# Optimization experiments

Measured on AMD Instinct MI355X. Metric: run time of the kernel, lower is better.

Reference implementation:

```python
import jax, jax.numpy as jnp
import numpy as np

T_ITERS = 48  # number of unrolled PDHG iterations (init kwarg T)


def _grad3(u):
    """Forward-difference gradient with circular BC.
    u: (P, 1, X, Y, T) -> (P, 3, X, Y, T).
    conv with kernel (0,-1,1) + circular pad == roll(v,-1,axis) - v."""
    v = u[:, 0]
    return jnp.stack([jnp.roll(v, -1, axis=a) - v for a in (1, 2, 3)], axis=1)


def _grad3_adj(q):
    """Adjoint (negative divergence) with circular BC.
    q: (P, 3, X, Y, T) -> (P, 1, X, Y, T)."""
    out = sum(jnp.roll(q[:, d], 1, axis=d + 1) - q[:, d] for d in range(3))
    return out[:, None]


def setup_inputs() -> dict:
    key = jax.random.key(0)
    k1, k2 = jax.random.split(key)
    x = jax.random.normal(k1, (2, 1, 160, 160, 16), dtype=jnp.float32)
    # positive per-voxel regularization map, one per gradient direction
    lambda_map = jax.random.uniform(k2, (2, 3, 160, 160, 16), dtype=jnp.float32)
    return {"x": x, "lambda_map": lambda_map}


def reference(x, lambda_map):
    # op_norm_AHA = 1, op_norm_GHG = sqrt(12) -> L = sqrt(1 + 12)
    L = jnp.sqrt(jnp.asarray(13.0, x.dtype))
    s10 = jax.nn.sigmoid(jnp.asarray(10.0, x.dtype))  # sigmoid of init value 10.0
    sigma = s10 / L
    tau = s10 / L
    theta = s10

    xnoisy = x
    p = x
    q = jnp.zeros((x.shape[0], 3) + x.shape[2:], dtype=x.dtype)
    x0 = x
    xbar = x

    def step(carry, _):
        p, q, x0, xbar = carry
        p = (p + sigma * (xbar - xnoisy)) / (1.0 + sigma)
        q = jnp.clip(q + sigma * _grad3(xbar), -lambda_map, lambda_map)
        x1 = x0 - tau * p - tau * _grad3_adj(q)
        xbar = x1 + theta * (x1 - x0)
        return (p, q, x1, xbar), None

    (p, q, x1, xbar), _ = jax.lax.scan(step, (p, q, x0, xbar), None, length=T_ITERS)
    return x1
```

## Files before the change

kernel.cpp:

```cpp
#include <hip/hip_runtime.h>
#include <math.h>

#define XDIM 160
#define YDIM 160
#define TDIM 16
#define NB 2
#define T_ITERS 48
#define TILE 10
#define R1S 16
#define R0S 18
#define TPT (XDIM / TILE)
#define NTHR 512
#define NTHRP 1024
#define NGRP (T_ITERS / 4)
#define FLAG_STRIDE 16

constexpr int VOL  = XDIM * YDIM * TDIM;
constexpr int NX   = NB * VOL;
constexpr int NBLK = NB * TPT * TPT;

constexpr int Q0B = R0S * R0S * TDIM;
constexpr int Q1B = Q0B + 17 * 16 * TDIM;
constexpr int SLDS = Q1B + 16 * 17 * TDIM;

typedef _Float16 hreal;
typedef _Float16 half4 __attribute__((ext_vector_type(4)));

__device__ __forceinline__ float clampl(float v, float l) {
    return fminf(fmaxf(v, -l), l);
}
__device__ __forceinline__ int wrap(int v) {
    return v < 0 ? v + XDIM : (v >= XDIM ? v - XDIM : v);
}
__device__ __forceinline__ int wrapT(int v) {
    return v < 0 ? v + TPT : (v >= TPT ? v - TPT : v);
}
__device__ __forceinline__ void ld4(const float* p, float* d) {
    float4 v = *(const float4*)p;
    d[0] = v.x; d[1] = v.y; d[2] = v.z; d[3] = v.w;
}
__device__ __forceinline__ void st4(float* p, const float* s) {
    *(float4*)p = make_float4(s[0], s[1], s[2], s[3]);
}
__device__ __forceinline__ void h2f4(const hreal* p, float* d) {
    half4 v = *(const half4*)p;
    d[0] = (float)v.x; d[1] = (float)v.y; d[2] = (float)v.z; d[3] = (float)v.w;
}
__device__ __forceinline__ float qrot_up(float x) {
    return __int_as_float(__builtin_amdgcn_update_dpp(
        0, __float_as_int(x), 0x39, 0xF, 0xF, true));
}
__device__ __forceinline__ float qrot_dn(float x) {
    return __int_as_float(__builtin_amdgcn_update_dpp(
        0, __float_as_int(x), 0x93, 0xF, 0xF, true));
}

__global__ __launch_bounds__(256) void init_kernel(
    const float* __restrict__ x, const float* __restrict__ lam,
    float* __restrict__ pA, float* __restrict__ xA,
    hreal* __restrict__ famA,
    hreal* __restrict__ lamh, hreal* __restrict__ xnh,
    unsigned* __restrict__ flags)
{
    int i = blockIdx.x * blockDim.x + threadIdx.x;
    if (i < NX) {
        float v = x[i];
        pA[i] = v; xA[i] = v;
        famA[i] = (hreal)v;
        xnh[i]  = (hreal)v;
    }
    if (i < 3 * NX) {
        famA[NX + i] = (hreal)0.f;
        lamh[i] = (hreal)lam[i];
    }
    if (flags && i < NBLK * FLAG_STRIDE) flags[i] = 0u;
}

__global__ __launch_bounds__(NTHRP, 8) void pd_persist(
    const hreal* __restrict__ xnh, const hreal* __restrict__ lamh,
    float* __restrict__ pA, float* __restrict__ pB,
    float* __restrict__ xA, float* __restrict__ xB,
    hreal* __restrict__ famA, hreal* __restrict__ famB,
    unsigned* __restrict__ flags,
    float sigma, float inv1ps, float tau, float theta)
{
    __shared__ float S[SLDS];

    const int tid = threadIdx.x;
    const int region = blockIdx.x & 7;
    const int local  = blockIdx.x >> 3;
    const int b  = region >> 2;
    const int tx = ((region >> 1) & 1) * 8 + (local >> 3);
    const int ty = (region & 1) * 8 + (local & 7);
    const int X0 = tx * TILE, Y0 = ty * TILE;
    const int t0 = (tid & 3) * 4;
    const int QD = NX + 2 * b * VOL;

    const int myFlag = (b * TPT * TPT + tx * TPT + ty) * FLAG_STRIDE;
    const unsigned* nbFlag = nullptr;
    if (tid < 8) {
        const int dxs[8] = {-1,-1,-1, 0, 0, 1, 1, 1};
        const int dys[8] = {-1, 0, 1,-1, 1,-1, 0, 1};
        int nx = wrapT(tx + dxs[tid]);
        int ny = wrapT(ty + dys[tid]);
        nbFlag = flags + (b * TPT * TPT + nx * TPT + ny) * FLAG_STRIDE;
    }

    const int line = tid >> 2;
    const int lx = line >> 4, ly = line & 15;

    float p[4], xv[4], q2[4];
    float xb[4], q0[4], q1[4];
    half4 XNr, L0r, L1r, L2r;

    const int gx0 = wrap(X0 - 3 + lx), gy0 = wrap(Y0 - 3 + ly);
    const int ro = b * VOL + (gx0 * YDIM + gy0) * TDIM + t0;
    const int so = b * VOL + ((X0 + lx - 3) * YDIM + (Y0 + ly - 3)) * TDIM + t0;
    const int a_xb  = ((lx + 1) * R0S + (ly + 1)) * TDIM + t0;
    const int a_q0w = Q0B + ((lx + 1) * 16 + ly) * TDIM + t0;
    const int a_q1w = Q1B + (lx * 17 + (ly + 1)) * TDIM + t0;
    const bool c_   = lx >= 3 && lx < 13 && ly >= 3 && ly < 13;
    const int ox = lx - 3, oy = ly - 3;
    const bool pxs_ = (ox >= 3 && ox < 7 && oy >= 3 && oy < 7);
    const bool qs_  = (ox >= 4 && ox < 6 && oy >= 4 && oy < 6);
    {
        int qoff = ro + 2 * b * VOL;
        XNr = *(const half4*)(xnh + ro);
        L0r = *(const half4*)(lamh + qoff);
        L1r = *(const half4*)(lamh + qoff + VOL);
        L2r = *(const half4*)(lamh + qoff + 2 * VOL);
    }
    half4 LRr;
    int rQ = 0, rXBC = 0;
    if (tid < 64) {
        int rly = tid >> 2;
        LRr = *(const half4*)(lamh + b * 3 * VOL +
              (wrap(X0 - 4) * YDIM + wrap(Y0 - 3 + rly)) * TDIM + t0);
        rQ   = Q0B + rly * TDIM + t0;
        rXBC = (rly + 1) * TDIM + t0;
    } else if (tid < 128) {
        int rlx = (tid - 64) >> 2;
        LRr = *(const half4*)(lamh + b * 3 * VOL + VOL +
              (wrap(X0 - 3 + rlx) * YDIM + wrap(Y0 - 4)) * TDIM + t0);
        rQ   = Q1B + (rlx * 17) * TDIM + t0;
        rXBC = ((rlx + 1) * R0S) * TDIM + t0;
    }

    #pragma unroll 1
    for (int g = 0; g < NGRP; ++g) {
        const bool e = (g & 1) == 0;
        const bool first = (g == 0);
        const bool fin   = (g == NGRP - 1);
        const float* __restrict__ pIn  = e ? pA : pB;
        float* __restrict__ pOut       = e ? pB : pA;
        const float* __restrict__ xIn  = e ? xA : xB;
        float* __restrict__ xOut       = e ? xB : xA;
        const hreal* __restrict__ famIn = e ? famA : famB;
        hreal* __restrict__ famOut      = e ? famB : famA;

        if (!first) {
            if (tid < 8) {
                const unsigned tgt = (unsigned)g;
                for (unsigned it = 0; it < (1u << 22); ++it) {
                    if (__hip_atomic_load(nbFlag, __ATOMIC_ACQUIRE,
                                          __HIP_MEMORY_SCOPE_AGENT) >= tgt)
                        break;
                    __builtin_amdgcn_s_sleep(1);
                }
            }
            __syncthreads();
            __threadfence();
        }

        for (int s = tid; s < R0S * R0S * 4; s += NTHRP) {
            int sq = s & 3, ln = s >> 2;
            int rx = ln / R0S, ry = ln % R0S;
            if (!first && rx >= 4 && rx < 14 && ry >= 4 && ry < 14) continue;
            int gx = wrap(X0 - 4 + rx), gy = wrap(Y0 - 4 + ry);
            float v[4];
            h2f4(famIn + b * VOL + (gx * YDIM + gy) * TDIM + sq * 4, v);
            st4(S + ln * TDIM + sq * 4, v);
        }
        for (int s = tid; s < 17 * 16 * 4; s += NTHRP) {
            int sq = s & 3, ln = s >> 2;
            int sx = ln / 16, sy = ln % 16;
            if (!first && sx >= 3 && sx < 14 && sy >= 3 && sy < 13) continue;
            int gx = wrap(X0 - 4 + sx), gy = wrap(Y0 - 3 + sy);
            float v[4];
            h2f4(famIn + NX + b * 3 * VOL + (gx * YDIM + gy) * TDIM + sq * 4, v);
            st4(S + Q0B + ln * TDIM + sq * 4, v);
        }
        for (int s = tid; s < 16 * 17 * 4; s += NTHRP) {
            int sq = s & 3, ln = s >> 2;
            int sx = ln / 17, sy = ln % 17;
            if (!first && sx >= 3 && sx < 13 && sy >= 3 && sy < 14) continue;
            int gx = wrap(X0 - 3 + sx), gy = wrap(Y0 - 4 + sy);
            float v[4];
            h2f4(famIn + NX + b * 3 * VOL + VOL + (gx * YDIM + gy) * TDIM + sq * 4, v);
            st4(S + Q1B + ln * TDIM + sq * 4, v);
        }

        if (first || !c_) {
            ld4(pIn + ro, p);
            ld4(xIn + ro, xv);
            h2f4(famIn + ro + QD + 2 * VOL, q2);
        }
        __syncthreads();

        ld4(S + a_xb, xb);

        #pragma unroll
        for (int k = 1; k <= 4; ++k) {
            const int lo = k - 1, hi = 17 - k;

            if (k == 1) {
                if (tid < 64) {
                    float qr[4], xbc[4], xpr[4];
                    ld4(S + rQ, qr);
                    ld4(S + rXBC, xbc);
                    ld4(S + rXBC + R0S * TDIM, xpr);
                    #pragma unroll
                    for (int j = 0; j < 4; ++j)
                        qr[j] = clampl(qr[j] + sigma * (xpr[j] - xbc[j]), (float)LRr[j]);
                    st4(S + rQ, qr);
                } else if (tid < 128) {
                    float qr[4], xbc[4], xpr[4];
                    ld4(S + rQ, qr);
                    ld4(S + rXBC, xbc);
                    ld4(S + rXBC + TDIM, xpr);
                    #pragma unroll
                    for (int j = 0; j < 4; ++j)
                        qr[j] = clampl(qr[j] + sigma * (xpr[j] - xbc[j]), (float)LRr[j]);
                    st4(S + rQ, qr);
                }
            }

            float xpx[4], xpy[4];
            if (k == 1) {
                ld4(S + a_q0w, q0);
                ld4(S + a_q1w, q1);
            }
            ld4(S + a_xb + R0S * TDIM, xpx);
            ld4(S + a_xb + TDIM,       xpy);
            {
                bool inX = (lx >= lo && lx < hi), inY = (ly >= lo && ly < hi);
                bool aq0 = inY && (lx >= lo - 1) && (lx < hi);
                bool aq1 = inX && (ly >= lo - 1) && (ly < hi);
                if (aq0) {
                    #pragma unroll
                    for (int j = 0; j < 4; ++j)
                        q0[j] = clampl(q0[j] + sigma * (xpx[j] - xb[j]),
                                       (float)L0r[j]);
                    st4(S + a_q0w, q0);
                }
                if (aq1) {
                    #pragma unroll
                    for (int j = 0; j < 4; ++j)
                        q1[j] = clampl(q1[j] + sigma * (xpy[j] - xb[j]),
                                       (float)L1r[j]);
                    st4(S + a_q1w, q1);
                }
            }
            __syncthreads();

            float q0b[4], q1b[4];
            ld4(S + a_q0w - 16 * TDIM, q0b);
            ld4(S + a_q1w - TDIM,      q1b);
            {
                bool ax = (lx >= lo && lx < hi && ly >= lo && ly < hi);
                if (ax) {
                    float xb_tp = qrot_up(xb[0]);
                    #pragma unroll
                    for (int j = 0; j < 4; ++j) {
                        float gt = ((j < 3) ? xb[j + 1] : xb_tp) - xb[j];
                        q2[j] = clampl(q2[j] + sigma * gt, (float)L2r[j]);
                        p[j]  = (p[j] + sigma * (xb[j] - (float)XNr[j]))
                                * inv1ps;
                    }

                    float q2tm = qrot_dn(q2[3]);
                    #pragma unroll
                    for (int j = 0; j < 4; ++j) {
                        float q2p = (j == 0) ? q2tm : q2[j - 1];
                        float div = (q0b[j] - q0[j]) + (q1b[j] - q1[j])
                                  + (q2p - q2[j]);
                        float xnew = xv[j] - tau * (p[j] + div);
                        xb[j] = xnew + theta * (xnew - xv[j]);
                        xv[j] = xnew;
                    }
                    st4(S + a_xb, xb);
                }
            }
            if (k < 4) __syncthreads();
        }

        if (c_) {
            if (fin) {
                st4(xOut + so, xv);
            } else {
                if (!pxs_) {
                    st4(pOut + so, p);
                    st4(xOut + so, xv);
                }
                if (!qs_) {
                    half4 h;
                    h.x = (hreal)xb[0]; h.y = (hreal)xb[1];
                    h.z = (hreal)xb[2]; h.w = (hreal)xb[3];
                    *(half4*)(famOut + so) = h;
                    h.x = (hreal)q0[0]; h.y = (hreal)q0[1];
                    h.z = (hreal)q0[2]; h.w = (hreal)q0[3];
                    *(half4*)(famOut + so + QD) = h;
                    h.x = (hreal)q1[0]; h.y = (hreal)q1[1];
                    h.z = (hreal)q1[2]; h.w = (hreal)q1[3];
                    *(half4*)(famOut + so + QD + VOL) = h;
                    h.x = (hreal)q2[0]; h.y = (hreal)q2[1];
                    h.z = (hreal)q2[2]; h.w = (hreal)q2[3];
                    *(half4*)(famOut + so + QD + 2 * VOL) = h;
                }
            }
        }

        if (!fin) {
            __threadfence();
            __syncthreads();
            if (tid == 0)
                __hip_atomic_store(flags + myFlag, (unsigned)(g + 1),
                                   __ATOMIC_RELEASE, __HIP_MEMORY_SCOPE_AGENT);
        }
    }
}

__global__ __launch_bounds__(NTHR, 4) void pd_step4(
    const hreal* __restrict__ xnh, const hreal* __restrict__ lamh,
    const float* __restrict__ pIn, float* __restrict__ pOut,
    const float* __restrict__ xIn, float* __restrict__ xOut,
    const hreal* __restrict__ xbIn, hreal* __restrict__ xbOut,
    const hreal* __restrict__ qIn, hreal* __restrict__ qOut,
    float sigma, float inv1ps, float tau, float theta)
{
    __shared__ float xbS[R0S * R0S * TDIM];
    __shared__ float q0S[17 * 16 * TDIM];
    __shared__ float q1S[16 * 17 * TDIM];

    const int tid = threadIdx.x;
    const int b   = blockIdx.x / (TPT * TPT);
    const int rem = blockIdx.x % (TPT * TPT);
    const int X0  = (rem / TPT) * TILE;
    const int Y0  = (rem % TPT) * TILE;
    const int xbase = b * VOL, qbase = b * 3 * VOL;

    const int qd = tid & 3, t0 = qd * 4;
    const int lane  = tid & 63;
    const int upSrc = (lane & 60) | ((lane + 1) & 3);
    const int dnSrc = (lane & 60) | ((lane + 3) & 3);

    for (int s = tid; s < R0S * R0S * 4; s += NTHR) {
        int sq = s & 3, ln = s >> 2;
        int rx = ln / R0S, ry = ln % R0S;
        int gx = wrap(X0 - 4 + rx), gy = wrap(Y0 - 4 + ry);
        float v[4];
        h2f4(xbIn + xbase + (gx * YDIM + gy) * TDIM + sq * 4, v);
        st4(xbS + ln * TDIM + sq * 4, v);
    }
    for (int s = tid; s < 17 * 16 * 4; s += NTHR) {
        int sq = s & 3, ln = s >> 2;
        int sx = ln / 16, sy = ln % 16;
        int gx = wrap(X0 - 4 + sx), gy = wrap(Y0 - 3 + sy);
        float v[4];
        h2f4(qIn + qbase + (gx * YDIM + gy) * TDIM + sq * 4, v);
        st4(q0S + ln * TDIM + sq * 4, v);
    }
    for (int s = tid; s < 16 * 17 * 4; s += NTHR) {
        int sq = s & 3, ln = s >> 2;
        int sx = ln / 17, sy = ln % 17;
        int gx = wrap(X0 - 3 + sx), gy = wrap(Y0 - 4 + sy);
        float v[4];
        h2f4(qIn + qbase + VOL + (gx * YDIM + gy) * TDIM + sq * 4, v);
        st4(q1S + ln * TDIM + sq * 4, v);
    }

    float p[2][4], xv[2][4], xb[2][4], q0[2][4], q1[2][4], q2[2][4];
    half4 XNr[2], L0r[2], L1r[2], L2r[2];
    #pragma unroll
    for (int m = 0; m < 2; ++m) {
        int line = 128 * m + (tid >> 2);
        int lx = line >> 4, ly = line & 15;
        int gx = wrap(X0 - 3 + lx), gy = wrap(Y0 - 3 + ly);
        int off  = xbase + (gx * YDIM + gy) * TDIM + t0;
        int qoff = qbase + (gx * YDIM + gy) * TDIM + t0;
        ld4(pIn + off, p[m]);
        ld4(xIn + off, xv[m]);
        h2f4(qIn + qoff + 2 * VOL, q2[m]);
        XNr[m] = *(const half4*)(xnh + off);
        L0r[m] = *(const half4*)(lamh + qoff);
        L1r[m] = *(const half4*)(lamh + qoff + VOL);
        L2r[m] = *(const half4*)(lamh + qoff + 2 * VOL);
    }

    half4 LRr;
    if (tid < 64) {
        int rly = tid >> 2;
        LRr = *(const half4*)(lamh + qbase +
              (wrap(X0 - 4) * YDIM + wrap(Y0 - 3 + rly)) * TDIM + t0);
    } else if (tid < 128) {
        int rlx = (tid - 64) >> 2;
        LRr = *(const half4*)(lamh + qbase + VOL +
              (wrap(X0 - 3 + rlx) * YDIM + wrap(Y0 - 4)) * TDIM + t0);
    }

    __syncthreads();

    #pragma unroll
    for (int m = 0; m < 2; ++m) {
        int line = 128 * m + (tid >> 2);
        int lx = line >> 4, ly = line & 15;
        ld4(xbS + ((lx + 1) * R0S + (ly + 1)) * TDIM + t0, xb[m]);
    }

    #pragma unroll
    for (int k = 1; k <= 4; ++k) {
        const int lo = k - 1, hi = 17 - k;

        if (k == 1) {
            if (tid < 64) {
                int rly = tid >> 2;
                float qr[4], xbc[4], xpx[4];
                ld4(q0S + rly * TDIM + t0, qr);
                ld4(xbS + (rly + 1) * TDIM + t0, xbc);
                ld4(xbS + (R0S + rly + 1) * TDIM + t0, xpx);
                #pragma unroll
                for (int j = 0; j < 4; ++j)
                    qr[j] = clampl(qr[j] + sigma * (xpx[j] - xbc[j]), (float)LRr[j]);
                st4(q0S + rly * TDIM + t0, qr);
            } else if (tid < 128) {
                int rlx = (tid - 64) >> 2;
                float qr[4], xbc[4], xpy[4];
                ld4(q1S + (rlx * 17) * TDIM + t0, qr);
                ld4(xbS + ((rlx + 1) * R0S) * TDIM + t0, xbc);
                ld4(xbS + ((rlx + 1) * R0S + 1) * TDIM + t0, xpy);
                #pragma unroll
                for (int j = 0; j < 4; ++j)
                    qr[j] = clampl(qr[j] + sigma * (xpy[j] - xbc[j]), (float)LRr[j]);
                st4(q1S + (rlx * 17) * TDIM + t0, qr);
            }
        }

        #pragma unroll
        for (int m = 0; m < 2; ++m) {
            int line = 128 * m + (tid >> 2);
            int lx = line >> 4, ly = line & 15;
            bool inX = (lx >= lo && lx < hi), inY = (ly >= lo && ly < hi);
            bool aq0 = inY && (lx >= lo - 1) && (lx < hi);
            bool aq1 = inX && (ly >= lo - 1) && (ly < hi);
            bool ax  = inX && inY;

            if (k == 1) {
                ld4(q0S + ((lx + 1) * 16 + ly) * TDIM + t0, q0[m]);
                ld4(q1S + (lx * 17 + (ly + 1)) * TDIM + t0, q1[m]);
            }
            if (aq0) {
                float xpx[4];
                ld4(xbS + ((lx + 2) * R0S + (ly + 1)) * TDIM + t0, xpx);
                #pragma unroll
                for (int j = 0; j < 4; ++j)
                    q0[m][j] = clampl(q0[m][j] + sigma * (xpx[j] - xb[m][j]),
                                      (float)L0r[m][j]);
                st4(q0S + ((lx + 1) * 16 + ly) * TDIM + t0, q0[m]);
            }
            if (aq1) {
                float xpy[4];
                ld4(xbS + ((lx + 1) * R0S + (ly + 2)) * TDIM + t0, xpy);
                #pragma unroll
                for (int j = 0; j < 4; ++j)
                    q1[m][j] = clampl(q1[m][j] + sigma * (xpy[j] - xb[m][j]),
                                      (float)L1r[m][j]);
                st4(q1S + (lx * 17 + (ly + 1)) * TDIM + t0, q1[m]);
            }
            if (ax) {
                float xb_tp = __shfl(xb[m][0], upSrc, 64);
                #pragma unroll
                for (int j = 0; j < 4; ++j) {
                    float gt = ((j < 3) ? xb[m][j + 1] : xb_tp) - xb[m][j];
                    q2[m][j] = clampl(q2[m][j] + sigma * gt, (float)L2r[m][j]);
                    p[m][j]  = (p[m][j] + sigma * (xb[m][j] - (float)XNr[m][j]))
                               * inv1ps;
                }
            }
        }
        __syncthreads();

        #pragma unroll
        for (int m = 0; m < 2; ++m) {
            int line = 128 * m + (tid >> 2);
            int lx = line >> 4, ly = line & 15;
            bool ax = (lx >= lo && lx < hi && ly >= lo && ly < hi);
            if (ax) {
                float q0b[4], q1b[4];
                ld4(q0S + (lx * 16 + ly) * TDIM + t0, q0b);
                ld4(q1S + (lx * 17 + ly) * TDIM + t0, q1b);
                float q2tm = __shfl(q2[m][3], dnSrc, 64);
                #pragma unroll
                for (int j = 0; j < 4; ++j) {
                    float q2p = (j == 0) ? q2tm : q2[m][j - 1];
                    float div = (q0b[j] - q0[m][j]) + (q1b[j] - q1[m][j])
                              + (q2p - q2[m][j]);
                    float xnew = xv[m][j] - tau * (p[m][j] + div);
                    xb[m][j] = xnew + theta * (xnew - xv[m][j]);
                    xv[m][j] = xnew;
                }
                if (k < 4)
                    st4(xbS + ((lx + 1) * R0S + (ly + 1)) * TDIM + t0, xb[m]);
            }
        }
        if (k < 4) __syncthreads();
    }

    #pragma unroll
    for (int m = 0; m < 2; ++m) {
        int line = 128 * m + (tid >> 2);
        int lx = line >> 4, ly = line & 15;
        if (lx >= 3 && lx < 13 && ly >= 3 && ly < 13) {
            int gx = X0 + lx - 3, gy = Y0 + ly - 3;
            int off  = xbase + (gx * YDIM + gy) * TDIM + t0;
            int qoff = qbase + (gx * YDIM + gy) * TDIM + t0;
            st4(pOut + off, p[m]);
            st4(xOut + off, xv[m]);
            half4 h;
            h.x = (hreal)xb[m][0]; h.y = (hreal)xb[m][1];
            h.z = (hreal)xb[m][2]; h.w = (hreal)xb[m][3];
            *(half4*)(xbOut + off) = h;
            h.x = (hreal)q0[m][0]; h.y = (hreal)q0[m][1];
            h.z = (hreal)q0[m][2]; h.w = (hreal)q0[m][3];
            *(half4*)(qOut + qoff) = h;
            h.x = (hreal)q1[m][0]; h.y = (hreal)q1[m][1];
            h.z = (hreal)q1[m][2]; h.w = (hreal)q1[m][3];
            *(half4*)(qOut + qoff + VOL) = h;
            h.x = (hreal)q2[m][0]; h.y = (hreal)q2[m][1];
            h.z = (hreal)q2[m][2]; h.w = (hreal)q2[m][3];
            *(half4*)(qOut + qoff + 2 * VOL) = h;
        }
    }
}

extern "C" void kernel_launch(void* const* d_in, const int* in_sizes, int n_in,
                              void* d_out, int out_size, void* d_ws, size_t ws_size,
                              hipStream_t stream) {
    const float* x   = (const float*)d_in[0];
    const float* lam = (const float*)d_in[1];
    float* out = (float*)d_out;
    float* ws  = (float*)d_ws;

    float* pA  = ws;
    float* pB  = ws + (size_t)NX;
    float* xBb = ws + (size_t)2 * NX;
    float* xAb = out;
    hreal* hb  = (hreal*)(ws + (size_t)3 * NX);
    hreal* famA = hb;
    hreal* famB = hb + (size_t)4 * NX;
    hreal* lamh = hb + (size_t)8 * NX;
    hreal* xnh  = hb + (size_t)11 * NX;
    unsigned* flags = (unsigned*)(ws + (size_t)9 * NX);

    const size_t ws_need = (size_t)9 * NX * sizeof(float)
                         + (size_t)NBLK * FLAG_STRIDE * sizeof(unsigned);

    const double s10 = 1.0 / (1.0 + exp(-10.0));
    const double L   = sqrt(13.0);
    float sigma  = (float)(s10 / L);
    float tau    = sigma;
    float theta  = (float)s10;
    float inv1ps = (float)(1.0 / (1.0 + s10 / L));

    static int persist_ok = -1;
    if (persist_ok < 0) {
        int nb = 0;
        hipError_t oe = hipOccupancyMaxActiveBlocksPerMultiprocessor(
            &nb, pd_persist, NTHRP, 0);
        persist_ok = (oe == hipSuccess && nb >= 2) ? 1 : 0;
        (void)hipGetLastError();
    }
    const bool use_persist = persist_ok == 1 && ws_size >= ws_need;

    init_kernel<<<(3 * NX + 255) / 256, 256, 0, stream>>>(
        x, lam, pA, xAb, famA, lamh, xnh, use_persist ? flags : nullptr);

    if (use_persist) {
        pd_persist<<<NBLK, NTHRP, 0, stream>>>(
            xnh, lamh, pA, pB, xAb, xBb, famA, famB, flags,
            sigma, inv1ps, tau, theta);
    } else {
        for (int j = 0; j < NGRP; ++j) {
            const bool e = (j & 1) == 0;
            pd_step4<<<NBLK, NTHR, 0, stream>>>(
                xnh, lamh,
                e ? pA : pB,   e ? pB : pA,
                e ? xAb : xBb, e ? xBb : xAb,
                e ? famA : famB, e ? famB : famA,
                e ? famA + NX : famB + NX, e ? famB + NX : famA + NX,
                sigma, inv1ps, tau, theta);
        }
    }
}
```

Measured before the change: 253.3 us.

## Recompute backward q neighbours in registers and double-buffer xbar to halve barriers

```diff
diff --git a/kernel.cpp b/kernel.cpp
--- a/kernel.cpp
+++ b/kernel.cpp
@@ -19,9 +19,8 @@
 constexpr int NX   = NB * VOL;
 constexpr int NBLK = NB * TPT * TPT;
 
-constexpr int Q0B = R0S * R0S * TDIM;
-constexpr int Q1B = Q0B + 17 * 16 * TDIM;
-constexpr int SLDS = Q1B + 16 * 17 * TDIM;
+constexpr int XBN  = R0S * R0S * TDIM;
+constexpr int SLDS = 2 * XBN;
 
 typedef _Float16 hreal;
 typedef _Float16 half4 __attribute__((ext_vector_type(4)));
@@ -85,6 +84,8 @@
     float sigma, float inv1ps, float tau, float theta)
 {
     __shared__ float S[SLDS];
+    float* const Sb0 = S;
+    float* const Sb1 = S + XBN;
 
     const int tid = threadIdx.x;
     const int region = blockIdx.x & 7;
@@ -109,17 +110,19 @@
     const int line = tid >> 2;
     const int lx = line >> 4, ly = line & 15;
 
-    float p[4], xv[4], q2[4];
-    float xb[4], q0[4], q1[4];
-    half4 XNr, L0r, L1r, L2r;
+    float p[4], xv[4], q2[4], xb[4], q0[4], q1[4], q0b[4], q1b[4];
+    half4 XNr, L0r, L1r, L2r, L0b, L1b;
 
     const int gx0 = wrap(X0 - 3 + lx), gy0 = wrap(Y0 - 3 + ly);
-    const int ro = b * VOL + (gx0 * YDIM + gy0) * TDIM + t0;
-    const int so = b * VOL + ((X0 + lx - 3) * YDIM + (Y0 + ly - 3)) * TDIM + t0;
-    const int a_xb  = ((lx + 1) * R0S + (ly + 1)) * TDIM + t0;
-    const int a_q0w = Q0B + ((lx + 1) * 16 + ly) * TDIM + t0;
-    const int a_q1w = Q1B + (lx * 17 + (ly + 1)) * TDIM + t0;
+    const int gxm = wrap(X0 - 4 + lx), gym = wrap(Y0 - 4 + ly);
+    const int ro   = b * VOL + (gx0 * YDIM + gy0) * TDIM + t0;
+    const int rob0 = b * VOL + (gxm * YDIM + gy0) * TDIM + t0;
+    const int rob1 = b * VOL + (gx0 * YDIM + gym) * TDIM + t0;
+    const int so   = b * VOL + ((X0 + lx - 3) * YDIM + (Y0 + ly - 3)) * TDIM + t0;
+    const int a_xb = ((lx + 1) * R0S + (ly + 1)) * TDIM + t0;
     const bool c_   = lx >= 3 && lx < 13 && ly >= 3 && ly < 13;
+    const bool cb0_ = lx >= 4 && lx < 14 && ly >= 3 && ly < 13;
+    const bool cb1_ = lx >= 3 && lx < 13 && ly >= 4 && ly < 14;
     const int ox = lx - 3, oy = ly - 3;
     const bool pxs_ = (ox >= 3 && ox < 7 && oy >= 3 && oy < 7);
     const bool qs_  = (ox >= 4 && ox < 6 && oy >= 4 && oy < 6);
@@ -129,21 +132,8 @@
         L0r = *(const half4*)(lamh + qoff);
         L1r = *(const half4*)(lamh + qoff + VOL);
         L2r = *(const half4*)(lamh + qoff + 2 * VOL);
-    }
-    half4 LRr;
-    int rQ = 0, rXBC = 0;
-    if (tid < 64) {
-        int rly = tid >> 2;
-        LRr = *(const half4*)(lamh + b * 3 * VOL +
-              (wrap(X0 - 4) * YDIM + wrap(Y0 - 3 + rly)) * TDIM + t0);
-        rQ   = Q0B + rly * TDIM + t0;
-        rXBC = (rly + 1) * TDIM + t0;
-    } else if (tid < 128) {
-        int rlx = (tid - 64) >> 2;
-        LRr = *(const half4*)(lamh + b * 3 * VOL + VOL +
-              (wrap(X0 - 3 + rlx) * YDIM + wrap(Y0 - 4)) * TDIM + t0);
-        rQ   = Q1B + (rlx * 17) * TDIM + t0;
-        rXBC = ((rlx + 1) * R0S) * TDIM + t0;
+        L0b = *(const half4*)(lamh + rob0 + 2 * b * VOL);
+        L1b = *(const half4*)(lamh + rob1 + 2 * b * VOL + VOL);
     }
 
     #pragma unroll 1
@@ -179,119 +169,82 @@
             int gx = wrap(X0 - 4 + rx), gy = wrap(Y0 - 4 + ry);
             float v[4];
             h2f4(famIn + b * VOL + (gx * YDIM + gy) * TDIM + sq * 4, v);
-            st4(S + ln * TDIM + sq * 4, v);
-        }
-        for (int s = tid; s < 17 * 16 * 4; s += NTHRP) {
-            int sq = s & 3, ln = s >> 2;
-            int sx = ln / 16, sy = ln % 16;
-            if (!first && sx >= 3 && sx < 14 && sy >= 3 && sy < 13) continue;
-            int gx = wrap(X0 - 4 + sx), gy = wrap(Y0 - 3 + sy);
-            float v[4];
-            h2f4(famIn + NX + b * 3 * VOL + (gx * YDIM + gy) * TDIM + sq * 4, v);
-            st4(S + Q0B + ln * TDIM + sq * 4, v);
-        }
-        for (int s = tid; s < 16 * 17 * 4; s += NTHRP) {
-            int sq = s & 3, ln = s >> 2;
-            int sx = ln / 17, sy = ln % 17;
-            if (!first && sx >= 3 && sx < 13 && sy >= 3 && sy < 14) continue;
-            int gx = wrap(X0 - 3 + sx), gy = wrap(Y0 - 4 + sy);
-            float v[4];
-            h2f4(famIn + NX + b * 3 * VOL + VOL + (gx * YDIM + gy) * TDIM + sq * 4, v);
-            st4(S + Q1B + ln * TDIM + sq * 4, v);
+            st4(Sb0 + ln * TDIM + sq * 4, v);
         }
 
         if (first || !c_) {
             ld4(pIn + ro, p);
             ld4(xIn + ro, xv);
             h2f4(famIn + ro + QD + 2 * VOL, q2);
-        }
+            h2f4(famIn + ro + QD,           q0);
+            h2f4(famIn + ro + QD + VOL,     q1);
+        }
+        if (first || !cb0_) h2f4(famIn + rob0 + QD,       q0b);
+        if (first || !cb1_) h2f4(famIn + rob1 + QD + VOL, q1b);
         __syncthreads();
 
-        ld4(S + a_xb, xb);
+        ld4(Sb0 + a_xb, xb);
 
         #pragma unroll
         for (int k = 1; k <= 4; ++k) {
             const int lo = k - 1, hi = 17 - k;
-
-            if (k == 1) {
-                if (tid < 64) {
-                    float qr[4], xbc[4], xpr[4];
-                    ld4(S + rQ, qr);
-                    ld4(S + rXBC, xbc);
-                    ld4(S + rXBC + R0S * TDIM, xpr);
-                    #pragma unroll
-                    for (int j = 0; j < 4; ++j)
-                        qr[j] = clampl(qr[j] + sigma * (xpr[j] - xbc[j]), (float)LRr[j]);
-                    st4(S + rQ, qr);
-                } else if (tid < 128) {
-                    float qr[4], xbc[4], xpr[4];
-                    ld4(S + rQ, qr);
-                    ld4(S + rXBC, xbc);
-                    ld4(S + rXBC + TDIM, xpr);
-                    #pragma unroll
-                    for (int j = 0; j < 4; ++j)
-                        qr[j] = clampl(qr[j] + sigma * (xpr[j] - xbc[j]), (float)LRr[j]);
-                    st4(S + rQ, qr);
-                }
-            }
-
-            float xpx[4], xpy[4];
-            if (k == 1) {
-                ld4(S + a_q0w, q0);
-                ld4(S + a_q1w, q1);
-            }
-            ld4(S + a_xb + R0S * TDIM, xpx);
-            ld4(S + a_xb + TDIM,       xpy);
-            {
-                bool inX = (lx >= lo && lx < hi), inY = (ly >= lo && ly < hi);
-                bool aq0 = inY && (lx >= lo - 1) && (lx < hi);
-                bool aq1 = inX && (ly >= lo - 1) && (ly < hi);
-                if (aq0) {
-                    #pragma unroll
-                    for (int j = 0; j < 4; ++j)
-                        q0[j] = clampl(q0[j] + sigma * (xpx[j] - xb[j]),
-                                       (float)L0r[j]);
-                    st4(S + a_q0w, q0);
-                }
-                if (aq1) {
-                    #pragma unroll
-                    for (int j = 0; j < 4; ++j)
-                        q1[j] = clampl(q1[j] + sigma * (xpy[j] - xb[j]),
-                                       (float)L1r[j]);
-                    st4(S + a_q1w, q1);
-                }
+            const float* rB = (k & 1) ? Sb0 : Sb1;
+            float*       wB = (k & 1) ? Sb1 : Sb0;
+
+            float xpx[4], xpy[4], xbm[4], xmy[4];
+            ld4(rB + a_xb + R0S * TDIM, xpx);
+            ld4(rB + a_xb + TDIM,       xpy);
+            ld4(rB + a_xb - R0S * TDIM, xbm);
+            ld4(rB + a_xb - TDIM,       xmy);
+
+            bool inX = (lx >= lo && lx < hi), inY = (ly >= lo && ly < hi);
+            bool aq0  = inY && (lx >= lo - 1) && (lx < hi);
+            bool aq1  = inX && (ly >= lo - 1) && (ly < hi);
+            bool aq0b = inY && (lx - 1 >= lo - 1) && (lx - 1 < hi);
+            bool aq1b = inX && (ly - 1 >= lo - 1) && (ly - 1 < hi);
+            bool ax   = inX && inY;
+
+            if (aq0) {
+                #pragma unroll
+                for (int j = 0; j < 4; ++j)
+                    q0[j] = clampl(q0[j] + sigma * (xpx[j] - xb[j]), (float)L0r[j]);
+            }
+            if (aq1) {
+                #pragma unroll
+                for (int j = 0; j < 4; ++j)
+                    q1[j] = clampl(q1[j] + sigma * (xpy[j] - xb[j]), (float)L1r[j]);
+            }
+            if (aq0b) {
+                #pragma unroll
+                for (int j = 0; j < 4; ++j)
+                    q0b[j] = clampl(q0b[j] + sigma * (xb[j] - xbm[j]), (float)L0b[j]);
+            }
+            if (aq1b) {
+                #pragma unroll
+                for (int j = 0; j < 4; ++j)
+                    q1b[j] = clampl(q1b[j] + sigma * (xb[j] - xmy[j]), (float)L1b[j]);
+            }
+            if (ax) {
+                float xb_tp = qrot_up(xb[0]);
+                #pragma unroll
+                for (int j = 0; j < 4; ++j) {
+                    float gt = ((j < 3) ? xb[j + 1] : xb_tp) - xb[j];
+                    q2[j] = clampl(q2[j] + sigma * gt, (float)L2r[j]);
+                    p[j]  = (p[j] + sigma * (xb[j] - (float)XNr[j])) * inv1ps;
+                }
+                float q2tm = qrot_dn(q2[3]);
+                #pragma unroll
+                for (int j = 0; j < 4; ++j) {
+                    float q2p = (j == 0) ? q2tm : q2[j - 1];
+                    float div = (q0b[j] - q0[j]) + (q1b[j] - q1[j])
+                              + (q2p - q2[j]);
+                    float xnew = xv[j] - tau * (p[j] + div);
+                    xb[j] = xnew + theta * (xnew - xv[j]);
+                    xv[j] = xnew;
+                }
+                st4(wB + a_xb, xb);
             }
             __syncthreads();
-
-            float q0b[4], q1b[4];
-            ld4(S + a_q0w - 16 * TDIM, q0b);
-            ld4(S + a_q1w - TDIM,      q1b);
-            {
-                bool ax = (lx >= lo && lx < hi && ly >= lo && ly < hi);
-                if (ax) {
-                    float xb_tp = qrot_up(xb[0]);
-                    #pragma unroll
-                    for (int j = 0; j < 4; ++j) {
-                        float gt = ((j < 3) ? xb[j + 1] : xb_tp) - xb[j];
-                        q2[j] = clampl(q2[j] + sigma * gt, (float)L2r[j]);
-                        p[j]  = (p[j] + sigma * (xb[j] - (float)XNr[j]))
-                                * inv1ps;
-                    }
-
-                    float q2tm = qrot_dn(q2[3]);
-                    #pragma unroll
-                    for (int j = 0; j < 4; ++j) {
-                        float q2p = (j == 0) ? q2tm : q2[j - 1];
-                        float div = (q0b[j] - q0[j]) + (q1b[j] - q1[j])
-                                  + (q2p - q2[j]);
-                        float xnew = xv[j] - tau * (p[j] + div);
-                        xb[j] = xnew + theta * (xnew - xv[j]);
-                        xv[j] = xnew;
-                    }
-                    st4(S + a_xb, xb);
-                }
-            }
-            if (k < 4) __syncthreads();
         }
 
         if (c_) {
```

Measured after the change: 253.8 us. Within noise of the previous version (+0.2%).
